# Kernel tuning notes

Hardware: AMD Instinct MI355X
Metric: run time of the kernel (lower is better)

The kernel has to match this reference:

```python
import jax, jax.numpy as jnp
import numpy as np

CLASS_NUM = 31
KERNEL_NUM = 5
KERNEL_MUL = 2.0


def setup_inputs() -> dict:
    key = jax.random.key(0)
    k1, k2, k3, k4 = jax.random.split(key, 4)
    B, D = 4096, 256
    source = jax.random.normal(k1, (B, D), dtype=jnp.float32)
    target = jax.random.normal(k2, (B, D), dtype=jnp.float32)
    s_label = jax.random.randint(k3, (B,), 0, CLASS_NUM, dtype=jnp.int64)
    t_label = jax.random.uniform(k4, (B, CLASS_NUM), dtype=jnp.float32)
    return {"source": source, "target": target, "s_label": s_label, "t_label": t_label}


def _cal_weight(s_label, t_label):
    # Source: one-hot, column-normalized (empty classes -> divide by 100)
    s_onehot = jax.nn.one_hot(s_label, CLASS_NUM, dtype=jnp.float32)
    s_cnt = jnp.sum(s_onehot, axis=0)
    s_vec = s_onehot / jnp.where(s_cnt == 0, 100.0, s_cnt)
    # Target: soft probs, column-normalized (detached in original)
    t_prob = jax.lax.stop_gradient(t_label)
    t_cnt = jnp.sum(t_prob, axis=0)
    t_vec = t_prob / jnp.where(t_cnt == 0, 100.0, t_cnt)
    # Classes present in BOTH source labels and target argmax predictions
    t_arg = jnp.argmax(t_prob, axis=1)
    t_present = jnp.sum(jax.nn.one_hot(t_arg, CLASS_NUM, dtype=jnp.float32), axis=0) > 0
    mask = ((s_cnt > 0) & t_present).astype(jnp.float32)
    n_idx = jnp.maximum(jnp.sum(mask), 1.0)
    s_vec = s_vec * mask
    t_vec = t_vec * mask
    w_ss = (s_vec @ s_vec.T) / n_idx
    w_tt = (t_vec @ t_vec.T) / n_idx
    w_st = (s_vec @ t_vec.T) / n_idx
    return w_ss, w_tt, w_st


def reference(source, target, s_label, t_label):
    B = source.shape[0]
    w_ss, w_tt, w_st = _cal_weight(s_label, t_label)

    # Multi-bandwidth RBF kernel over concatenated samples
    total = jnp.concatenate([source, target], axis=0)  # [2B, D]
    sq = jnp.sum(total * total, axis=1)
    l2 = jnp.maximum(sq[:, None] + sq[None, :] - 2.0 * (total @ total.T), 0.0)  # [2B, 2B]

    n = 2 * B
    bw = jnp.sum(jax.lax.stop_gradient(l2)) / float(max(n * n - n, 1))
    bw = jnp.maximum(bw, 1e-6) / (KERNEL_MUL ** (KERNEL_NUM // 2))
    kernels = jnp.zeros_like(l2)
    for i in range(KERNEL_NUM):
        kernels = kernels + jnp.exp(-l2 / jnp.maximum(bw * KERNEL_MUL ** i, 1e-6))

    ss = kernels[:B, :B]
    tt = kernels[B:, B:]
    st = kernels[:B, B:]
    loss = jnp.sum(w_ss * ss + w_tt * tt - 2.0 * w_st * st)
    return loss
```

## Files before the change

### kernel.cpp

```cpp
#include <hip/hip_runtime.h>
#include <cstddef>


#define B 4096
#define D 256
#define C 31
#define N2 8192
#define NTILE 64
#define NBLK (NTILE * (NTILE + 1) / 2)

typedef __attribute__((ext_vector_type(8))) short bf16x8;
typedef __attribute__((ext_vector_type(4))) float f32x4;

struct WS {
  double sum_sq;
  double Msum[256];
  int s_cnt[32];
  float t_cnt[32];
  int t_pres[32];
  float inv_n_idx;
  float inv_d4;
  float sq[N2];
  int slab[N2];
  float sdv[N2];
  alignas(16) unsigned char Thi8[(size_t)N2 * D];
  alignas(16) unsigned short vhi[(size_t)N2 * 32];
  alignas(16) float v[(size_t)N2 * 32];
  alignas(16) double part[NBLK];
};

static __device__ __forceinline__ unsigned short f2bf(float f) {
  unsigned int u = __float_as_uint(f);
  return (unsigned short)((u + 0x7fffu + ((u >> 16) & 1u)) >> 16);
}
static __device__ __forceinline__ float bf2f(unsigned short s) {
  return __uint_as_float(((unsigned int)s) << 16);
}

#define GLD16(gsrc, ldst)                                                     \
  __builtin_amdgcn_global_load_lds(                                           \
      (const __attribute__((address_space(1))) void*)(gsrc),                  \
      (__attribute__((address_space(3))) void*)(ldst), 16, 0, 0)

__global__ void k0_init(WS* __restrict__ ws) {
  int tid = threadIdx.x;
  if (tid == 0) ws->sum_sq = 0.0;
  if (tid < 32) {
    ws->s_cnt[tid] = 0;
    ws->t_cnt[tid] = 0.f;
    ws->t_pres[tid] = 0;
  }
  ws->Msum[tid] = 0.0;
}

__global__ __launch_bounds__(256) void kPrep(const float* __restrict__ src,
                                             const float* __restrict__ tgt,
                                             const int* __restrict__ s_label,
                                             const float* __restrict__ t_label,
                                             WS* __restrict__ ws) {
  int tid = threadIdx.x, w = tid >> 6, lane = tid & 63;
  int r0 = blockIdx.x * 32;
  bool is_src = (r0 < B);
  __shared__ float rsq[32];
  __shared__ float colp[4][256];
  __shared__ int ls[32];
  __shared__ float lt[8][32];
  __shared__ int lpres[32];
  if (tid < 32) { ls[tid] = 0; lpres[tid] = 0; }

  const float* basep =
      is_src ? src + (size_t)r0 * D : tgt + (size_t)(r0 - B) * D;

  float4 xv[8];
#pragma unroll
  for (int i = 0; i < 8; ++i)
    xv[i] = *(const float4*)(basep + (size_t)(w * 8 + i) * D + lane * 4);

  float ca0 = 0.f, ca1 = 0.f, ca2 = 0.f, ca3 = 0.f;
  int sc = lane >> 4, gl = (lane >> 1) & 7, hf = lane & 1;
#pragma unroll
  for (int i = 0; i < 8; ++i) {
    int rr = w * 8 + i;
    int p = r0 + rr;
    float4 x = xv[i];
    unsigned int pk = __builtin_amdgcn_cvt_pk_fp8_f32(x.x, x.y, 0, false);
    pk = __builtin_amdgcn_cvt_pk_fp8_f32(x.z, x.w, pk, true);
    int gp = (gl + p + (p >> 1)) & 7;
    *(unsigned int*)(&ws->Thi8[(size_t)p * D + sc * 64 + gp * 8 + hf * 4]) = pk;
    ca0 += x.x; ca1 += x.y; ca2 += x.z; ca3 += x.w;
    float s = x.x * x.x + x.y * x.y + x.z * x.z + x.w * x.w;
#pragma unroll
    for (int off = 32; off; off >>= 1) s += __shfl_down(s, off, 64);
    if (lane == 0) rsq[rr] = s;
  }
  colp[w][lane * 4 + 0] = ca0;
  colp[w][lane * 4 + 1] = ca1;
  colp[w][lane * 4 + 2] = ca2;
  colp[w][lane * 4 + 3] = ca3;

  if (!is_src) {
    int g = tid >> 5, c = tid & 31;
    float s = 0.f;
    if (c < C) {
#pragma unroll
      for (int k = 0; k < 4; ++k)
        s += t_label[(size_t)(r0 - B + g * 4 + k) * C + c];
    }
    lt[g][c] = s;
    int rr = tid >> 3, j = tid & 7;
    float best = -1e30f;
    int barg = 0;
    for (int c2 = j; c2 < C; c2 += 8) {
      float x = t_label[(size_t)(r0 - B + rr) * C + c2];
      if (x > best) { best = x; barg = c2; }
    }
#pragma unroll
    for (int m = 1; m < 8; m <<= 1) {
      float ob = __shfl_xor(best, m, 64);
      int oa = __shfl_xor(barg, m, 64);
      if (ob > best || (ob == best && oa < barg)) { best = ob; barg = oa; }
    }
    if (j == 0) lpres[barg] = 1;
  }
  __syncthreads();

  if (tid < 32) {
    int p = r0 + tid;
    ws->sq[p] = rsq[tid];
    if (is_src) {
      int lb = s_label[p];
      ws->slab[p] = lb;
      atomicAdd(&ls[lb], 1);
    } else {
      ws->slab[p] = 0;
    }
  }
  if (tid < 64) {
    float ss = (tid < 32) ? rsq[tid] : 0.f;
#pragma unroll
    for (int off = 32; off; off >>= 1) ss += __shfl_down(ss, off, 64);
    if (tid == 0) atomicAdd(&ws->sum_sq, (double)ss);
  }
  atomicAdd(&ws->Msum[tid],
            (double)(colp[0][tid] + colp[1][tid] + colp[2][tid] + colp[3][tid]));
  __syncthreads();
  if (tid < 32) {
    if (is_src) {
      if (ls[tid]) atomicAdd(&ws->s_cnt[tid], ls[tid]);
    } else {
      float s = 0.f;
#pragma unroll
      for (int g = 0; g < 8; ++g) s += lt[g][tid];
      atomicAdd(&ws->t_cnt[tid], s);
      if (lpres[tid]) ws->t_pres[tid] = 1;
    }
  }
}

__global__ __launch_bounds__(256) void kFin(const int* __restrict__ s_label,
                                            const float* __restrict__ t_label,
                                            WS* __restrict__ ws) {
  int tid = threadIdx.x;
  __shared__ float sdiv[32], tdiv[32];
  if (tid < 64) {
    int m = 0;
    if (tid < 32) {
      int cnt = ws->s_cnt[tid];
      m = (tid < C) && (cnt > 0) && (ws->t_pres[tid] != 0);
      sdiv[tid] = m ? 1.f / (float)cnt : 0.f;
      float t = ws->t_cnt[tid];
      tdiv[tid] = m ? 1.f / ((t == 0.f) ? 100.f : t) : 0.f;
    }
    unsigned long long bal = __ballot(m);
    if (tid == 0 && blockIdx.x == 0)
      ws->inv_n_idx = 1.f / fmaxf((float)__popcll(bal), 1.f);
  } else if (tid < 128 && blockIdx.x == 0) {
    int lane = tid - 64;
    double msq = 0.0;
#pragma unroll
    for (int i = 0; i < 4; ++i) {
      double mm = ws->Msum[i * 64 + lane];
      msq += mm * mm;
    }
#pragma unroll
    for (int off = 32; off; off >>= 1) msq += __shfl_down(msq, off, 64);
    if (lane == 0) {
      double S = ws->sum_sq;
      double n = (double)N2;
      double sum_l2 = 2.0 * n * S - 2.0 * msq;
      double bw = sum_l2 / (n * n - n);
      bw = fmax(bw, 1e-6) * 0.25;
      ws->inv_d4 = (float)(1.0 / fmax(bw * 16.0, 1e-6));
    }
  }
  __syncthreads();
  int p = blockIdx.x * 256 + tid;
  float vrow[32];
  if (p < B) {
    int lb = s_label[p];
    float sv = sdiv[lb];
    ws->sdv[p] = sv;
#pragma unroll
    for (int c = 0; c < 32; ++c) vrow[c] = (c == lb) ? sv : 0.f;
  } else {
    ws->sdv[p] = 0.f;
    const float* r = t_label + (size_t)(p - B) * C;
#pragma unroll
    for (int c = 0; c < 32; ++c) vrow[c] = (c < C) ? -r[c] * tdiv[c] : 0.f;
  }
#pragma unroll
  for (int k = 0; k < 8; ++k) {
    float4 vf;
    vf.x = vrow[k * 4 + 0]; vf.y = vrow[k * 4 + 1];
    vf.z = vrow[k * 4 + 2]; vf.w = vrow[k * 4 + 3];
    *(float4*)(&ws->v[(size_t)p * 32 + k * 4]) = vf;
    ushort4 vh;
    vh.x = f2bf(vf.x); vh.y = f2bf(vf.y); vh.z = f2bf(vf.z); vh.w = f2bf(vf.w);
    *(ushort4*)(&ws->vhi[(size_t)p * 32 + k * 4]) = vh;
  }
}

template <int KIND, bool DIAG>
static __device__ __forceinline__ float epi_ss_st(
    const f32x4 (&acc)[4][4], float cinv, const float* tSq, const int* tSlab,
    const float* tSdv, const unsigned short* Vsw, int p0, int q0, int wr,
    int wc, int mrow, int quad) {
  float k2 = 2.f * cinv;
  float cq[4], sdq[4];
  int lq[4];
#pragma unroll
  for (int tj = 0; tj < 4; ++tj) {
    int iq = 128 + wc + tj * 16 + mrow;
    cq[tj] = -cinv * tSq[iq];
    if (KIND == 0) {
      lq[tj] = tSlab[iq];
      sdq[tj] = tSdv[iq];
    }
  }
  float local = 0.f;
#pragma unroll
  for (int ti = 0; ti < 4; ++ti) {
#pragma unroll
    for (int rg = 0; rg < 4; ++rg) {
      int ip = wr + ti * 16 + quad * 4 + rg;
      float cpl = -cinv * tSq[ip];
      int lp = tSlab[ip];
      float sp = tSdv[ip];
#pragma unroll
      for (int tj = 0; tj < 4; ++tj) {
        float z = fminf(fmaf(k2, acc[ti][tj][rg], cpl + cq[tj]), 0.f);
        float y = __expf(z);
        float kv = y;
        y *= y; kv += y;
        y *= y; kv += y;
        y *= y; kv += y;
        y *= y; kv += y;
        float wv;
        if (KIND == 0) {
          wv = (lp == lq[tj]) ? sp * sdq[tj] : 0.f;
        } else {
          int ql = wc + tj * 16 + mrow;
          wv = sp * bf2f(Vsw[ql * 32 + ((lp + ql) & 31)]);
        }
        if (DIAG) {
          int p = p0 + ip;
          int q = q0 + wc + tj * 16 + mrow;
          float f = (q > p) ? 2.f : ((q == p) ? 1.f : 0.f);
          local = fmaf(wv * f, kv, local);
        } else {
          local = fmaf(wv, kv, local);
        }
      }
    }
  }
  if (!DIAG) local *= 2.f;
  return local;
}

template <bool DIAG>
static __device__ __forceinline__ float epi_tt(const f32x4 (&acc)[4][4],
                                               float cinv, const float* tSq,
                                               const unsigned short* SA,
                                               const unsigned short* SB,
                                               int p0, int q0, int wr, int wc,
                                               int mrow, int quad) {
  float k2 = 2.f * cinv;
  float cq[4];
#pragma unroll
  for (int tj = 0; tj < 4; ++tj)
    cq[tj] = -cinv * tSq[128 + wc + tj * 16 + mrow];
  float cp[16];
#pragma unroll
  for (int ti = 0; ti < 4; ++ti)
#pragma unroll
    for (int rg = 0; rg < 4; ++rg)
      cp[ti * 4 + rg] = -cinv * tSq[wr + ti * 16 + quad * 4 + rg];
  bf16x8 af[4], bfr[4];
#pragma unroll
  for (int ti = 0; ti < 4; ++ti)
    af[ti] = *(const bf16x8*)(SA + (wr + ti * 16 + mrow) * 32 + quad * 8);
#pragma unroll
  for (int tj = 0; tj < 4; ++tj)
    bfr[tj] = *(const bf16x8*)(SB + (wc + tj * 16 + mrow) * 32 + quad * 8);
  float local = 0.f;
#pragma unroll
  for (int ti = 0; ti < 4; ++ti) {
#pragma unroll
    for (int tj = 0; tj < 4; ++tj) {
      f32x4 wv4 = __builtin_amdgcn_mfma_f32_16x16x32_bf16(
          af[ti], bfr[tj], (f32x4){0.f, 0.f, 0.f, 0.f}, 0, 0, 0);
#pragma unroll
      for (int rg = 0; rg < 4; ++rg) {
        float z = fminf(fmaf(k2, acc[ti][tj][rg], cp[ti * 4 + rg] + cq[tj]), 0.f);
        float y = __expf(z);
        float kv = y;
        y *= y; kv += y;
        y *= y; kv += y;
        y *= y; kv += y;
        y *= y; kv += y;
        if (DIAG) {
          int p = p0 + wr + ti * 16 + quad * 4 + rg;
          int q = q0 + wc + tj * 16 + mrow;
          float f = (q > p) ? 2.f : ((q == p) ? 1.f : 0.f);
          local = fmaf(wv4[rg] * f, kv, local);
        } else {
          local = fmaf(wv4[rg], kv, local);
        }
      }
    }
  }
  if (!DIAG) local *= 2.f;
  return local;
}

__global__ __launch_bounds__(256, 3) void k3_main(WS* __restrict__ ws) {
  int tid = threadIdx.x, w = tid >> 6, lane = tid & 63;
  int lin0 = blockIdx.x;
  int e = (lin0 & 7) * (NBLK / 8) + (lin0 >> 3);
  int b = 0, nb = 484, rem = e;
  while (rem >= nb) { rem -= nb; ++b; nb -= 64; }
  int base = b * 8;
  int bq_, r;
  if (rem < 36) {
    bq_ = 0;
    while ((bq_ + 1) * (bq_ + 2) / 2 <= rem) ++bq_;
    r = rem - (bq_ * (bq_ + 1)) / 2;
  } else {
    int t = rem - 36;
    bq_ = 8 + (t >> 3);
    r = t & 7;
  }
  int bp = base + r, bq = base + bq_;
  int p0 = bp * 128, q0 = bq * 128;

  bool is_ss = (bq < 32);
  bool is_tt = (bp >= 32);
  bool is_st = !is_ss && !is_tt;

  __shared__ __align__(16) unsigned char S[2][2][8192];
  __shared__ __align__(16) float tSq[256];
  __shared__ __align__(16) int tSlab[256];
  __shared__ __align__(16) float tSdv[256];
  unsigned short* Vsw = (unsigned short*)&S[0][0][0];
  unsigned short* SA = (unsigned short*)&S[0][0][0];
  unsigned short* SB = (unsigned short*)&S[0][1][0];
  double* red = (double*)&S[1][0][0];

  const int wr = (w >> 1) * 64, wc = (w & 1) * 64;
  const int mrow = lane & 15, quad = lane >> 4;
  f32x4 acc[4][4];
#pragma unroll
  for (int i = 0; i < 4; ++i)
#pragma unroll
    for (int j = 0; j < 4; ++j) acc[i][j] = (f32x4){0.f, 0.f, 0.f, 0.f};

  const unsigned char* T8 = ws->Thi8;
  int rA = tid >> 2, cb16 = (tid & 3) * 16, cp8 = (tid & 3) * 8;
  const unsigned char* a_lo = T8 + (size_t)(p0 + rA) * D + cb16;
  const unsigned char* a_hi = a_lo + (size_t)64 * D;
  const unsigned char* b_lo = T8 + (size_t)(q0 + rA) * D + cb16;
  const unsigned char* b_hi = b_lo + (size_t)64 * D;

#define STAGE(bufi, off)                                                      \
  do {                                                                        \
    GLD16(a_lo + (off), &S[bufi][0][w * 1024]);                               \
    GLD16(a_hi + (off), &S[bufi][0][w * 1024 + 4096]);                        \
    GLD16(b_lo + (off), &S[bufi][1][w * 1024]);                               \
    GLD16(b_hi + (off), &S[bufi][1][w * 1024 + 4096]);                        \
  } while (0)

  int aAdr[4], bAdr[4];
#pragma unroll
  for (int ti = 0; ti < 4; ++ti) {
    int Ra = wr + ti * 16 + mrow;
    aAdr[ti] = Ra * 64 + (((quad + Ra + (Ra >> 1)) & 7) << 3);
    int Rb = wc + ti * 16 + mrow;
    bAdr[ti] = Rb * 64 + (((quad + Rb + (Rb >> 1)) & 7) << 3);
  }

  uint4 stv0 = {0, 0, 0, 0}, stv1 = {0, 0, 0, 0};

  STAGE(0, 0);
  __syncthreads();

#pragma unroll
  for (int i = 0; i < 4; ++i) {
    const int bufi = i & 1;
    if (i < 3) STAGE(bufi ^ 1, (i + 1) * 64);
    if (i == 0 && w == 0) {
      int l32 = lane & 31;
      const float* s1 = ((lane < 32) ? ws->sq + p0 : ws->sq + q0) + l32 * 4;
      GLD16(s1, tSq);
      const int* s2 = ((lane < 32) ? ws->slab + p0 : ws->slab + q0) + l32 * 4;
      GLD16(s2, tSlab);
      const float* s3 = ((lane < 32) ? ws->sdv + p0 : ws->sdv + q0) + l32 * 4;
      GLD16(s3, tSdv);
    }
    if (i == 2 && is_st) {
      const uint4* vsrc = (const uint4*)(ws->vhi +
                                         (size_t)(q0 + (tid >> 1)) * 32 +
                                         (tid & 1) * 16);
      stv0 = vsrc[0];
      stv1 = vsrc[1];
    }
    if (i == 3 && is_tt) {
      const unsigned short* gA = ws->vhi + (size_t)(p0 + rA) * 32 + cp8;
      const unsigned short* gB = ws->vhi + (size_t)(q0 + rA) * 32 + cp8;
      GLD16(gA, &S[0][0][w * 1024]);
      GLD16(gA + (size_t)64 * 32, &S[0][0][w * 1024 + 4096]);
      GLD16(gB, &S[0][1][w * 1024]);
      GLD16(gB + (size_t)64 * 32, &S[0][1][w * 1024 + 4096]);
    }
    const unsigned char* fb = &S[bufi][0][0];
#pragma unroll
    for (int t = 0; t < 2; ++t) {
      const int x = t << 5;
      long aF[4], bF[4];
#pragma unroll
      for (int ti = 0; ti < 4; ++ti)
        aF[ti] = *(const long*)(fb + (aAdr[ti] ^ x));
#pragma unroll
      for (int tj = 0; tj < 4; ++tj)
        bF[tj] = *(const long*)(fb + 8192 + (bAdr[tj] ^ x));
#pragma unroll
      for (int ti = 0; ti < 4; ++ti)
#pragma unroll
        for (int tj = 0; tj < 4; ++tj)
          acc[ti][tj] = __builtin_amdgcn_mfma_f32_16x16x32_fp8_fp8(
              aF[ti], bF[tj], acc[ti][tj], 0, 0, 0);
    }
    if (i < 3) __syncthreads();
  }

  if (is_st) {
    int rr = tid >> 1, h = (tid & 1) * 16;
    unsigned int uu[8] = {stv0.x, stv0.y, stv0.z, stv0.w,
                          stv1.x, stv1.y, stv1.z, stv1.w};
#pragma unroll
    for (int j = 0; j < 8; ++j) {
      Vsw[rr * 32 + ((h + 2 * j + rr) & 31)] = (unsigned short)(uu[j] & 0xffff);
      Vsw[rr * 32 + ((h + 2 * j + 1 + rr) & 31)] = (unsigned short)(uu[j] >> 16);
    }
  }
  __syncthreads();

  float cinv = ws->inv_d4;
  float local;
  if (is_ss) {
    if (bp == bq)
      local = epi_ss_st<0, true>(acc, cinv, tSq, tSlab, tSdv, Vsw, p0, q0, wr,
                                 wc, mrow, quad);
    else
      local = epi_ss_st<0, false>(acc, cinv, tSq, tSlab, tSdv, Vsw, p0, q0, wr,
                                  wc, mrow, quad);
  } else if (is_st) {
    local = epi_ss_st<1, false>(acc, cinv, tSq, tSlab, tSdv, Vsw, p0, q0, wr,
                                wc, mrow, quad);
  } else {
    if (bp == bq)
      local = epi_tt<true>(acc, cinv, tSq, SA, SB, p0, q0, wr, wc, mrow, quad);
    else
      local = epi_tt<false>(acc, cinv, tSq, SA, SB, p0, q0, wr, wc, mrow, quad);
  }

  double dl = (double)local;
#pragma unroll
  for (int off = 32; off; off >>= 1) dl += __shfl_down(dl, off, 64);
  if (lane == 0) red[w] = dl;
  __syncthreads();
  if (tid == 0) ws->part[lin0] = red[0] + red[1] + red[2] + red[3];
#undef STAGE
}

__global__ __launch_bounds__(256) void k4_out(WS* __restrict__ ws,
                                              float* __restrict__ out) {
  __shared__ double sh[4];
  int tid = threadIdx.x, w = tid >> 6, lane = tid & 63;
  double s = 0.0;
  for (int i = tid; i < NBLK; i += 256) s += ws->part[i];
#pragma unroll
  for (int off = 32; off; off >>= 1) s += __shfl_down(s, off, 64);
  if (lane == 0) sh[w] = s;
  __syncthreads();
  if (tid == 0)
    out[0] = (float)((sh[0] + sh[1] + sh[2] + sh[3]) * (double)ws->inv_n_idx);
}

extern "C" void kernel_launch(void* const* d_in, const int* in_sizes, int n_in,
                              void* d_out, int out_size, void* d_ws, size_t ws_size,
                              hipStream_t stream) {
  const float* src = (const float*)d_in[0];
  const float* tgt = (const float*)d_in[1];
  const int* s_label = (const int*)d_in[2];
  const float* t_label = (const float*)d_in[3];
  float* out = (float*)d_out;
  WS* ws = (WS*)d_ws;

  k0_init<<<1, 256, 0, stream>>>(ws);
  kPrep<<<256, 256, 0, stream>>>(src, tgt, s_label, t_label, ws);
  kFin<<<32, 256, 0, stream>>>(s_label, t_label, ws);
  k3_main<<<NBLK, 256, 0, stream>>>(ws);
  k4_out<<<1, 256, 0, stream>>>(ws, out);
}
```

Before: 116.9 us.

## Triple-buffer K-loop with vmcnt-gated barriers and use hardware exp2 in epilogue

Replaces the double-buffered four-chunk fp8 MFMA loop with a three-buffer LDS pipeline. Each barrier waits only on the loads it needs, using explicit s_waitcnt vmcnt counts, so prefetches stay in flight across compute. The epilogue folds log2(e) into the scale constant and calls v_exp_f32 directly instead of __expf, removing a multiply per element. This costs more shared memory, which may reduce occupancy, and the hand-counted vmcnt values are fragile if the compiler reorders or adds memory operations.

```diff
diff --git a/kernel.cpp b/kernel.cpp
--- a/kernel.cpp
+++ b/kernel.cpp
@@ -36,6 +36,11 @@
 static __device__ __forceinline__ float bf2f(unsigned short s) {
   return __uint_as_float(((unsigned int)s) << 16);
 }
+static __device__ __forceinline__ float exp2_hw(float x) {
+  float r;
+  asm("v_exp_f32 %0, %1" : "=v"(r) : "v"(x));
+  return r;
+}
 
 #define GLD16(gsrc, ldst)                                                     \
   __builtin_amdgcn_global_load_lds(                                           \
@@ -222,16 +227,16 @@
 
 template <int KIND, bool DIAG>
 static __device__ __forceinline__ float epi_ss_st(
-    const f32x4 (&acc)[4][4], float cinv, const float* tSq, const int* tSlab,
+    const f32x4 (&acc)[4][4], float ci2, const float* tSq, const int* tSlab,
     const float* tSdv, const unsigned short* Vsw, int p0, int q0, int wr,
     int wc, int mrow, int quad) {
-  float k2 = 2.f * cinv;
+  float k2 = 2.f * ci2;
   float cq[4], sdq[4];
   int lq[4];
 #pragma unroll
   for (int tj = 0; tj < 4; ++tj) {
     int iq = 128 + wc + tj * 16 + mrow;
-    cq[tj] = -cinv * tSq[iq];
+    cq[tj] = -ci2 * tSq[iq];
     if (KIND == 0) {
       lq[tj] = tSlab[iq];
       sdq[tj] = tSdv[iq];
@@ -243,13 +248,13 @@
 #pragma unroll
     for (int rg = 0; rg < 4; ++rg) {
       int ip = wr + ti * 16 + quad * 4 + rg;
-      float cpl = -cinv * tSq[ip];
+      float cpl = -ci2 * tSq[ip];
       int lp = tSlab[ip];
       float sp = tSdv[ip];
 #pragma unroll
       for (int tj = 0; tj < 4; ++tj) {
         float z = fminf(fmaf(k2, acc[ti][tj][rg], cpl + cq[tj]), 0.f);
-        float y = __expf(z);
+        float y = exp2_hw(z);
         float kv = y;
         y *= y; kv += y;
         y *= y; kv += y;
@@ -279,22 +284,22 @@
 
 template <bool DIAG>
 static __device__ __forceinline__ float epi_tt(const f32x4 (&acc)[4][4],
-                                               float cinv, const float* tSq,
+                                               float ci2, const float* tSq,
                                                const unsigned short* SA,
                                                const unsigned short* SB,
                                                int p0, int q0, int wr, int wc,
                                                int mrow, int quad) {
-  float k2 = 2.f * cinv;
+  float k2 = 2.f * ci2;
   float cq[4];
 #pragma unroll
   for (int tj = 0; tj < 4; ++tj)
-    cq[tj] = -cinv * tSq[128 + wc + tj * 16 + mrow];
+    cq[tj] = -ci2 * tSq[128 + wc + tj * 16 + mrow];
   float cp[16];
 #pragma unroll
   for (int ti = 0; ti < 4; ++ti)
 #pragma unroll
     for (int rg = 0; rg < 4; ++rg)
-      cp[ti * 4 + rg] = -cinv * tSq[wr + ti * 16 + quad * 4 + rg];
+      cp[ti * 4 + rg] = -ci2 * tSq[wr + ti * 16 + quad * 4 + rg];
   bf16x8 af[4], bfr[4];
 #pragma unroll
   for (int ti = 0; ti < 4; ++ti)
@@ -312,7 +317,7 @@
 #pragma unroll
       for (int rg = 0; rg < 4; ++rg) {
         float z = fminf(fmaf(k2, acc[ti][tj][rg], cp[ti * 4 + rg] + cq[tj]), 0.f);
-        float y = __expf(z);
+        float y = exp2_hw(z);
         float kv = y;
         y *= y; kv += y;
         y *= y; kv += y;
@@ -332,6 +337,36 @@
   if (!DIAG) local *= 2.f;
   return local;
 }
+
+static __device__ __forceinline__ void do_chunk(const unsigned char* fb,
+                                                f32x4 (&acc)[4][4],
+                                                const int (&aAdr)[4],
+                                                const int (&bAdr)[4]) {
+#pragma unroll
+  for (int t = 0; t < 2; ++t) {
+    const int x = t << 5;
+    long aF[4], bF[4];
+#pragma unroll
+    for (int ti = 0; ti < 4; ++ti)
+      aF[ti] = *(const long*)(fb + (aAdr[ti] ^ x));
+#pragma unroll
+    for (int tj = 0; tj < 4; ++tj)
+      bF[tj] = *(const long*)(fb + 8192 + (bAdr[tj] ^ x));
+#pragma unroll
+    for (int ti = 0; ti < 4; ++ti)
+#pragma unroll
+      for (int tj = 0; tj < 4; ++tj)
+        acc[ti][tj] = __builtin_amdgcn_mfma_f32_16x16x32_fp8_fp8(
+            aF[ti], bF[tj], acc[ti][tj], 0, 0, 0);
+  }
+}
+
+#define WBAR(N)                                                               \
+  do {                                                                        \
+    asm volatile("s_waitcnt vmcnt(" #N ")" ::: "memory");                     \
+    __builtin_amdgcn_s_barrier();                                             \
+    asm volatile("" ::: "memory");                                            \
+  } while (0)
 
 __global__ __launch_bounds__(256, 3) void k3_main(WS* __restrict__ ws) {
   int tid = threadIdx.x, w = tid >> 6, lane = tid & 63;
@@ -357,14 +392,14 @@
   bool is_tt = (bp >= 32);
   bool is_st = !is_ss && !is_tt;
 
-  __shared__ __align__(16) unsigned char S[2][2][8192];
+  __shared__ __align__(16) unsigned char S[3][2][8192];
   __shared__ __align__(16) float tSq[256];
   __shared__ __align__(16) int tSlab[256];
   __shared__ __align__(16) float tSdv[256];
-  unsigned short* Vsw = (unsigned short*)&S[0][0][0];
-  unsigned short* SA = (unsigned short*)&S[0][0][0];
-  unsigned short* SB = (unsigned short*)&S[0][1][0];
-  double* red = (double*)&S[1][0][0];
+  unsigned short* Vsw = (unsigned short*)&S[1][0][0];
+  unsigned short* SA = (unsigned short*)&S[1][0][0];
+  unsigned short* SB = (unsigned short*)&S[1][1][0];
+  double* red = (double*)&S[2][0][0];
 
   const int wr = (w >> 1) * 64, wc = (w & 1) * 64;
   const int mrow = lane & 15, quad = lane >> 4;
@@ -401,56 +436,48 @@
   uint4 stv0 = {0, 0, 0, 0}, stv1 = {0, 0, 0, 0};
 
   STAGE(0, 0);
-  __syncthreads();
-
-#pragma unroll
-  for (int i = 0; i < 4; ++i) {
-    const int bufi = i & 1;
-    if (i < 3) STAGE(bufi ^ 1, (i + 1) * 64);
-    if (i == 0 && w == 0) {
-      int l32 = lane & 31;
-      const float* s1 = ((lane < 32) ? ws->sq + p0 : ws->sq + q0) + l32 * 4;
-      GLD16(s1, tSq);
-      const int* s2 = ((lane < 32) ? ws->slab + p0 : ws->slab + q0) + l32 * 4;
-      GLD16(s2, tSlab);
-      const float* s3 = ((lane < 32) ? ws->sdv + p0 : ws->sdv + q0) + l32 * 4;
-      GLD16(s3, tSdv);
-    }
-    if (i == 2 && is_st) {
-      const uint4* vsrc = (const uint4*)(ws->vhi +
-                                         (size_t)(q0 + (tid >> 1)) * 32 +
-                                         (tid & 1) * 16);
-      stv0 = vsrc[0];
-      stv1 = vsrc[1];
-    }
-    if (i == 3 && is_tt) {
-      const unsigned short* gA = ws->vhi + (size_t)(p0 + rA) * 32 + cp8;
-      const unsigned short* gB = ws->vhi + (size_t)(q0 + rA) * 32 + cp8;
-      GLD16(gA, &S[0][0][w * 1024]);
-      GLD16(gA + (size_t)64 * 32, &S[0][0][w * 1024 + 4096]);
-      GLD16(gB, &S[0][1][w * 1024]);
-      GLD16(gB + (size_t)64 * 32, &S[0][1][w * 1024 + 4096]);
-    }
-    const unsigned char* fb = &S[bufi][0][0];
-#pragma unroll
-    for (int t = 0; t < 2; ++t) {
-      const int x = t << 5;
-      long aF[4], bF[4];
-#pragma unroll
-      for (int ti = 0; ti < 4; ++ti)
-        aF[ti] = *(const long*)(fb + (aAdr[ti] ^ x));
-#pragma unroll
-      for (int tj = 0; tj < 4; ++tj)
-        bF[tj] = *(const long*)(fb + 8192 + (bAdr[tj] ^ x));
-#pragma unroll
-      for (int ti = 0; ti < 4; ++ti)
-#pragma unroll
-        for (int tj = 0; tj < 4; ++tj)
-          acc[ti][tj] = __builtin_amdgcn_mfma_f32_16x16x32_fp8_fp8(
-              aF[ti], bF[tj], acc[ti][tj], 0, 0, 0);
-    }
-    if (i < 3) __syncthreads();
-  }
+  STAGE(1, 64);
+  {
+    int l32 = lane & 31;
+    const float* s1 = ((lane < 32) ? ws->sq + p0 : ws->sq + q0) + l32 * 4;
+    GLD16(s1, tSq);
+    const int* s2 = ((lane < 32) ? ws->slab + p0 : ws->slab + q0) + l32 * 4;
+    GLD16(s2, tSlab);
+    const float* s3 = ((lane < 32) ? ws->sdv + p0 : ws->sdv + q0) + l32 * 4;
+    GLD16(s3, tSdv);
+  }
+  WBAR(7);
+
+  STAGE(2, 128);
+  do_chunk(&S[0][0][0], acc, aAdr, bAdr);
+  WBAR(7);
+
+  STAGE(0, 192);
+  do_chunk(&S[1][0][0], acc, aAdr, bAdr);
+  WBAR(4);
+
+  if (is_st) {
+    const uint4* vsrc = (const uint4*)(ws->vhi + (size_t)(q0 + (tid >> 1)) * 32 +
+                                       (tid & 1) * 16);
+    stv0 = vsrc[0];
+    stv1 = vsrc[1];
+  }
+  do_chunk(&S[2][0][0], acc, aAdr, bAdr);
+  if (is_st) {
+    WBAR(2);
+  } else {
+    WBAR(0);
+  }
+
+  if (is_tt) {
+    const unsigned short* gA = ws->vhi + (size_t)(p0 + rA) * 32 + cp8;
+    const unsigned short* gB = ws->vhi + (size_t)(q0 + rA) * 32 + cp8;
+    GLD16(gA, &S[1][0][w * 1024]);
+    GLD16(gA + (size_t)64 * 32, &S[1][0][w * 1024 + 4096]);
+    GLD16(gB, &S[1][1][w * 1024]);
+    GLD16(gB + (size_t)64 * 32, &S[1][1][w * 1024 + 4096]);
+  }
+  do_chunk(&S[0][0][0], acc, aAdr, bAdr);
 
   if (is_st) {
     int rr = tid >> 1, h = (tid & 1) * 16;
@@ -464,23 +491,23 @@
   }
   __syncthreads();
 
-  float cinv = ws->inv_d4;
+  float ci2 = ws->inv_d4 * 1.44269504f;
   float local;
   if (is_ss) {
     if (bp == bq)
-      local = epi_ss_st<0, true>(acc, cinv, tSq, tSlab, tSdv, Vsw, p0, q0, wr,
+      local = epi_ss_st<0, true>(acc, ci2, tSq, tSlab, tSdv, Vsw, p0, q0, wr,
                                  wc, mrow, quad);
     else
-      local = epi_ss_st<0, false>(acc, cinv, tSq, tSlab, tSdv, Vsw, p0, q0, wr,
+      local = epi_ss_st<0, false>(acc, ci2, tSq, tSlab, tSdv, Vsw, p0, q0, wr,
                                   wc, mrow, quad);
   } else if (is_st) {
-    local = epi_ss_st<1, false>(acc, cinv, tSq, tSlab, tSdv, Vsw, p0, q0, wr,
+    local = epi_ss_st<1, false>(acc, ci2, tSq, tSlab, tSdv, Vsw, p0, q0, wr,
                                 wc, mrow, quad);
   } else {
     if (bp == bq)
-      local = epi_tt<true>(acc, cinv, tSq, SA, SB, p0, q0, wr, wc, mrow, quad);
+      local = epi_tt<true>(acc, ci2, tSq, SA, SB, p0, q0, wr, wc, mrow, quad);
     else
-      local = epi_tt<false>(acc, cinv, tSq, SA, SB, p0, q0, wr, wc, mrow, quad);
+      local = epi_tt<false>(acc, ci2, tSq, SA, SB, p0, q0, wr, wc, mrow, quad);
   }
 
   double dl = (double)local;
```

Measured after the change: 115.2 us. No clear change (-1.5%).
